# Performance work log

Measured on AMD Instinct MI355X. Metric: run time of the kernel, lower is better.

## Reference

```python
import math
import jax, jax.numpy as jnp
import numpy as np

B, T, E = 4, 2048, 768
H, D = 3, E // 3  # 3 heads, head_dim = emb_sz // 3
USE_MASK = True


def setup_inputs() -> dict:
    key = jax.random.key(0)
    ks = jax.random.split(key, 8)
    s_in = 1.0 / math.sqrt(E)
    return {
        "inputs_for_keys": jax.random.normal(ks[0], (B, T, E), jnp.float32),
        "inputs_for_values": jax.random.normal(ks[1], (B, T, E), jnp.float32),
        "inputs_for_queries": jax.random.normal(ks[2], (B, T, E), jnp.float32),
        # per-head projection weights, stacked over head axis: [H, E, D]
        "Wk": jax.random.normal(ks[3], (H, E, D), jnp.float32) * s_in,
        "Wq": jax.random.normal(ks[4], (H, E, D), jnp.float32) * s_in,
        "Wv": jax.random.normal(ks[5], (H, E, D), jnp.float32) * s_in,
        # final Dense(emb_sz)
        "Wo": jax.random.normal(ks[6], (E, E), jnp.float32) * s_in,
        "bo": jnp.zeros((E,), jnp.float32),
    }


def reference(inputs_for_keys, inputs_for_values, inputs_for_queries, Wk, Wq, Wv, Wo, bo):
    # Project per head: [B,T,E] x [H,E,D] -> [B,H,T,D]
    K = jnp.einsum('bte,hed->bhtd', inputs_for_keys, Wk)
    V = jnp.einsum('bte,hed->bhtd', inputs_for_values, Wv)
    Q = jnp.einsum('bte,hed->bhtd', inputs_for_queries, Wq)
    # NOTE: original scales by sqrt(window_size_keys) = sqrt(T), not sqrt(D)
    scores = jnp.einsum('bhqd,bhkd->bhqk', Q, K) / math.sqrt(T)
    if USE_MASK:
        mask = jnp.triu(jnp.full((T, T), -jnp.inf, dtype=scores.dtype), k=1)
        scores = scores + mask
    attn = jax.nn.softmax(scores, axis=-1)  # [B,H,Tq,Tk]
    z = jnp.einsum('bhqk,bhkd->bhqd', attn, V)  # [B,H,T,D]
    # concat heads in order head1,head2,head3 along last axis -> [B,T,E]
    z = jnp.transpose(z, (0, 2, 1, 3)).reshape(B, T, H * D)
    return z @ Wo + bo
```

## Files before the change

### kernel.cpp

```cpp
#include <hip/hip_runtime.h>
#include <hip/hip_bf16.h>
#include <math.h>

#define B_ 4
#define T_ 2048
#define E_ 768
#define H_ 3
#define D_ 256
#define LOG2E 1.4426950408889634f

typedef __attribute__((ext_vector_type(8))) _Float16 half8;
typedef __attribute__((ext_vector_type(8))) unsigned short ushort8;
typedef __attribute__((ext_vector_type(4))) float f32x4;

static __device__ inline unsigned short f2h(float x) {
    _Float16 h = (_Float16)x;
    return *reinterpret_cast<unsigned short*>(&h);
}

#define GLOAD_LDS(SRC, DST) \
    __builtin_amdgcn_global_load_lds( \
        (const __attribute__((address_space(1))) void*)(SRC), \
        (__attribute__((address_space(3))) void*)(DST), 16, 0, 0)

__global__ __launch_bounds__(256)
void transpose_cast_all(const float* __restrict__ Wk, const float* __restrict__ Wq,
                        const float* __restrict__ Wv, const float* __restrict__ Wo,
                        unsigned short* __restrict__ WTk, unsigned short* __restrict__ WTq,
                        unsigned short* __restrict__ WTv, unsigned short* __restrict__ WoT)
{
    __shared__ float tile[32][33];
    const int z = blockIdx.z;
    const float* in; unsigned short* out; int R, C;
    if (z < 9) {
        const int mat = z / 3, hd = z % 3;
        R = E_; C = D_;
        in  = (mat == 0 ? Wk  : mat == 1 ? Wq  : Wv)  + (long)hd * E_ * D_;
        out = (mat == 0 ? WTk : mat == 1 ? WTq : WTv) + (long)hd * D_ * E_;
    } else {
        R = E_; C = E_;
        in = Wo; out = WoT;
    }
    const int c0 = blockIdx.x * 32;
    const int r0 = blockIdx.y * 32;
    if (c0 >= C) return;
    const int t  = threadIdx.x;
    const int cc = t & 31, rr = t >> 5;
    #pragma unroll
    for (int i = 0; i < 4; ++i)
        tile[rr + i * 8][cc] = in[(long)(r0 + rr + i * 8) * C + c0 + cc];
    __syncthreads();
    const int rr2 = t & 31, cc2 = t >> 5;
    #pragma unroll
    for (int i = 0; i < 4; ++i)
        out[(long)(c0 + cc2 + i * 8) * R + r0 + rr2] = f2h(tile[rr2][cc2 + i * 8]);
}

__global__ __launch_bounds__(256)
void transpose16(const unsigned short* __restrict__ in, unsigned short* __restrict__ out,
                 int R, int Ccols)
{
    __shared__ unsigned short tile[64 * 64];
    char* tb = (char*)tile;
    const long zoff = (long)blockIdx.z * R * Ccols;
    const int r0 = blockIdx.y * 64, c0 = blockIdx.x * 64;
    const int t = threadIdx.x;
    #pragma unroll
    for (int i = 0; i < 2; ++i) {
        const int rr = (t >> 3) + i * 32;
        const int gc = (t & 7) * 8;
        ushort8 v = *(const ushort8*)(in + zoff + (long)(r0 + rr) * Ccols + c0 + gc);
        *(ushort8*)(tb + rr * 128 + ((gc * 2) ^ (((rr >> 3) & 7) << 4))) = v;
    }
    __syncthreads();
    #pragma unroll
    for (int i = 0; i < 2; ++i) {
        const int cc = (t >> 3) + i * 32;
        const int gr = (t & 7) * 8;
        ushort8 v;
        #pragma unroll
        for (int e = 0; e < 8; ++e) {
            const int row = gr + e;
            v[e] = *(const unsigned short*)(tb + row * 128 + ((cc * 2) ^ (((row >> 3) & 7) << 4)));
        }
        *(ushort8*)(out + zoff + (long)(c0 + cc) * R + r0 + gr) = v;
    }
}

template<bool CONVA, bool OUT16>
__device__ __forceinline__
void gemm_body(const float* Af, const unsigned short* Ah, const unsigned short* Bz,
               void* Cz, const float* bias, int K, int lda, int ldc,
               int m0, int n0, int tid)
{
    __shared__ unsigned short As[128 * 32];
    __shared__ unsigned short Bs[128 * 32];

    const int lane = tid & 63, wid = tid >> 6;
    const int wm = wid >> 1, wn = wid & 1;
    const int fr = lane & 15, fg = lane >> 4;

    f32x4 acc[4][4];
    #pragma unroll
    for (int mt = 0; mt < 4; ++mt)
        #pragma unroll
        for (int nt = 0; nt < 4; ++nt) acc[mt][nt] = (f32x4)(0.f);

    for (int k0 = 0; k0 < K; k0 += 32) {
        #pragma unroll
        for (int i = 0; i < 2; ++i) {
            const int G = tid + i * 256;
            const int row = G >> 2, g = G & 3;
            ushort8 pa;
            if (CONVA) {
                const float* s = Af + (long)(m0 + row) * lda + k0 + g * 8;
                float4 f0 = *(const float4*)s, f1 = *(const float4*)(s + 4);
                pa[0] = f2h(f0.x); pa[1] = f2h(f0.y); pa[2] = f2h(f0.z); pa[3] = f2h(f0.w);
                pa[4] = f2h(f1.x); pa[5] = f2h(f1.y); pa[6] = f2h(f1.z); pa[7] = f2h(f1.w);
            } else {
                pa = *(const ushort8*)(Ah + (long)(m0 + row) * lda + k0 + g * 8);
            }
            *(ushort8*)&As[row * 32 + g * 8] = pa;
            *(ushort8*)&Bs[row * 32 + g * 8] =
                *(const ushort8*)(Bz + (long)(n0 + row) * K + k0 + g * 8);
        }
        __syncthreads();

        half8 a[4], b[4];
        #pragma unroll
        for (int mt = 0; mt < 4; ++mt)
            a[mt] = *(const half8*)&As[(wm * 64 + mt * 16 + fr) * 32 + fg * 8];
        #pragma unroll
        for (int nt = 0; nt < 4; ++nt)
            b[nt] = *(const half8*)&Bs[(wn * 64 + nt * 16 + fr) * 32 + fg * 8];
        #pragma unroll
        for (int mt = 0; mt < 4; ++mt)
            #pragma unroll
            for (int nt = 0; nt < 4; ++nt)
                acc[mt][nt] = __builtin_amdgcn_mfma_f32_16x16x32_f16(
                                  a[mt], b[nt], acc[mt][nt], 0, 0, 0);
        __syncthreads();
    }

    #pragma unroll
    for (int nt = 0; nt < 4; ++nt) {
        const int col = n0 + wn * 64 + nt * 16 + fr;
        const float badd = bias ? bias[col] : 0.f;
        #pragma unroll
        for (int mt = 0; mt < 4; ++mt) {
            const int row = m0 + wm * 64 + mt * 16 + fg * 4;
            #pragma unroll
            for (int reg = 0; reg < 4; ++reg) {
                if (OUT16)
                    ((unsigned short*)Cz)[(long)(row + reg) * ldc + col] =
                        f2h(acc[mt][nt][reg] + badd);
                else
                    ((float*)Cz)[(long)(row + reg) * ldc + col] =
                        acc[mt][nt][reg] + badd;
            }
        }
    }
}

template<bool CONVA, bool OUT16>
__global__ __launch_bounds__(256)
void gemm_mfma(const void* __restrict__ Av, const unsigned short* __restrict__ Bt,
               void* __restrict__ Cv, const float* __restrict__ bias,
               int K, int Hdiv, int lda, int ldc, long sA, long sB, long sC)
{
    const int z = blockIdx.z;
    const float*          Af = (const float*)Av          + (long)(z / Hdiv) * sA;
    const unsigned short* Ah = (const unsigned short*)Av + (long)(z / Hdiv) * sA;
    const unsigned short* Bz = Bt + (long)(z % Hdiv) * sB;
    void* Cz = OUT16 ? (void*)((unsigned short*)Cv + (long)z * sC)
                     : (void*)((float*)Cv + (long)z * sC);
    gemm_body<CONVA, OUT16>(Af, Ah, Bz, Cz, bias, K, lda, ldc,
                            blockIdx.y * 128, blockIdx.x * 128, threadIdx.x);
}

__global__ __launch_bounds__(256)
void qkv_proj(const float* __restrict__ Xk, const float* __restrict__ Xv,
              const float* __restrict__ Xq,
              const unsigned short* __restrict__ WTk, const unsigned short* __restrict__ WTv,
              const unsigned short* __restrict__ WTq,
              unsigned short* __restrict__ Kp, unsigned short* __restrict__ Vp,
              unsigned short* __restrict__ Qp)
{
    const int z = blockIdx.z;
    const int which = z / 12, bh = z % 12;
    const int b = bh / H_, h = bh % H_;
    const float* X = (which == 0) ? Xk : (which == 1) ? Xv : Xq;
    const unsigned short* W = (which == 0) ? WTk : (which == 1) ? WTv : WTq;
    unsigned short* P = (which == 0) ? Kp : (which == 1) ? Vp : Qp;
    const float* Af = X + (long)b * T_ * E_;
    const unsigned short* Bz = W + (long)h * D_ * E_;
    unsigned short* Cz = P + (long)bh * T_ * D_;
    gemm_body<true, true>(Af, nullptr, Bz, Cz, nullptr, E_, E_, D_,
                          blockIdx.y * 128, blockIdx.x * 128, threadIdx.x);
}

__global__ __launch_bounds__(256, 2)
void flash_lds(const unsigned short* __restrict__ Qb, const unsigned short* __restrict__ Kb,
               const unsigned short* __restrict__ Vtb, unsigned short* __restrict__ Z2h,
               float scale_log2e)
{
    __shared__ unsigned short Ktile[2][32 * 256];
    __shared__ unsigned short Vtile[2][256 * 32];
    __shared__ unsigned short Ps[4][16 * 72];

    const int p  = blockIdx.x;
    const int bh = p % 12;
    const int pi = p / 12;
    const int qtB = 63 - pi;
    const int b = bh / H_, h = bh % H_;
    const int tid = threadIdx.x;
    const int w = tid >> 6, lane = tid & 63;
    const int g = lane >> 4, fr = lane & 15;
    const int qw0 = (w < 2) ? (pi * 32 + w * 16) : (qtB * 32 + (w - 2) * 16);

    const unsigned short* kg = Kb  + (long)bh * T_ * D_;
    const unsigned short* vg = Vtb + (long)bh * D_ * T_;

    const unsigned short* qrow = Qb + ((long)bh * T_ + qw0 + fr) * D_;
    const _Float16 hs = (_Float16)scale_log2e;
    half8 qf[8];
    #pragma unroll
    for (int c = 0; c < 8; ++c) {
        qf[c] = *(const half8*)(qrow + c * 32 + g * 8);
        qf[c] *= hs;
    }

    f32x4 o[16];
    #pragma unroll
    for (int dt = 0; dt < 16; ++dt) o[dt] = (f32x4)(0.f);
    float mrow[4] = {-INFINITY, -INFINITY, -INFINITY, -INFINITY};
    float lrow[4] = {0.f, 0.f, 0.f, 0.f};

    const int nkt = qtB + 1;

    auto STAGE = [&](int bufi, int kt) {
        const int k0 = kt * 32;
        #pragma unroll
        for (int i = 0; i < 4; ++i) {
            const int L = tid + i * 256;
            const int r = L >> 5, cg = L & 31;
            GLOAD_LDS(kg + (long)(k0 + r) * D_ + ((cg ^ (r & 7)) * 8),
                      &Ktile[bufi][L * 8]);
        }
        #pragma unroll
        for (int i = 0; i < 4; ++i) {
            const int L = tid + i * 256;
            const int dr = L >> 2, gq = L & 3;
            GLOAD_LDS(vg + (long)dr * T_ + k0 + ((gq ^ ((dr >> 1) & 3)) * 8),
                      &Vtile[bufi][L * 8]);
        }
    };

    STAGE(0, 0);
    int buf = 0;
    for (int kt = 0; kt < nkt; ++kt) {
        const bool pf = (kt + 1 < nkt);
        if (pf) {
            STAGE(buf ^ 1, kt + 1);
            asm volatile("s_waitcnt vmcnt(8)" ::: "memory");
        } else {
            asm volatile("s_waitcnt vmcnt(0)" ::: "memory");
        }
        __builtin_amdgcn_sched_barrier(0);
        __builtin_amdgcn_s_barrier();
        __builtin_amdgcn_sched_barrier(0);

        const int k0 = kt * 32;
        if (k0 <= qw0 + 15) {
            f32x4 s[2];
            s[0] = (f32x4)(0.f); s[1] = (f32x4)(0.f);
            const int kkey = fr & 7;
            __builtin_amdgcn_s_setprio(1);
            #pragma unroll
            for (int c = 0; c < 8; ++c) {
                #pragma unroll
                for (int nt = 0; nt < 2; ++nt) {
                    const int kr = nt * 16 + fr;
                    half8 kf = *(const half8*)&Ktile[buf][(kr * 32 + ((c * 4 + g) ^ kkey)) * 8];
                    s[nt] = __builtin_amdgcn_mfma_f32_16x16x32_f16(qf[c], kf, s[nt], 0, 0, 0);
                }
            }
            __builtin_amdgcn_s_setprio(0);

            const bool diag = (k0 + 31 > qw0);
            float sv[2][4];
            #pragma unroll
            for (int nt = 0; nt < 2; ++nt)
                #pragma unroll
                for (int reg = 0; reg < 4; ++reg) {
                    float v = s[nt][reg];
                    if (diag && (k0 + nt * 16 + fr > qw0 + g * 4 + reg)) v = -INFINITY;
                    sv[nt][reg] = v;
                }

            float pmax[4];
            #pragma unroll
            for (int reg = 0; reg < 4; ++reg) pmax[reg] = fmaxf(sv[0][reg], sv[1][reg]);
            const bool ok = (pmax[0] <= mrow[0] + 8.f) && (pmax[1] <= mrow[1] + 8.f)
                         && (pmax[2] <= mrow[2] + 8.f) && (pmax[3] <= mrow[3] + 8.f);
            if (!__all(ok)) {
                #pragma unroll
                for (int reg = 0; reg < 4; ++reg) {
                    float tm = pmax[reg];
                    tm = fmaxf(tm, __shfl_xor(tm, 1));
                    tm = fmaxf(tm, __shfl_xor(tm, 2));
                    tm = fmaxf(tm, __shfl_xor(tm, 4));
                    tm = fmaxf(tm, __shfl_xor(tm, 8));
                    const float mnew = fmaxf(mrow[reg], tm);
                    const float alpha = exp2f(mrow[reg] - mnew);
                    mrow[reg] = mnew;
                    lrow[reg] *= alpha;
                    #pragma unroll
                    for (int dt = 0; dt < 16; ++dt) o[dt][reg] *= alpha;
                }
            }
            #pragma unroll
            for (int nt = 0; nt < 2; ++nt)
                #pragma unroll
                for (int reg = 0; reg < 4; ++reg) {
                    const float pp = exp2f(sv[nt][reg] - mrow[reg]);
                    lrow[reg] += pp;
                    Ps[w][(g * 4 + reg) * 72 + nt * 16 + fr] = f2h(pp);
                }

            const half8 pf0 = *(const half8*)&Ps[w][fr * 72 + g * 8];

            const int vkey = g ^ ((fr >> 1) & 3);
            __builtin_amdgcn_s_setprio(1);
            #pragma unroll
            for (int dt = 0; dt < 16; ++dt) {
                const int dr = dt * 16 + fr;
                half8 vf = *(const half8*)&Vtile[buf][(dr * 4 + vkey) * 8];
                o[dt] = __builtin_amdgcn_mfma_f32_16x16x32_f16(pf0, vf, o[dt], 0, 0, 0);
            }
            __builtin_amdgcn_s_setprio(0);
        }
        __builtin_amdgcn_sched_barrier(0);
        __builtin_amdgcn_s_barrier();
        buf ^= 1;
    }

    float inv[4];
    #pragma unroll
    for (int reg = 0; reg < 4; ++reg) {
        float ps = lrow[reg];
        ps += __shfl_xor(ps, 1);
        ps += __shfl_xor(ps, 2);
        ps += __shfl_xor(ps, 4);
        ps += __shfl_xor(ps, 8);
        inv[reg] = 1.f / ps;
    }
    const long rowbase = ((long)b * T_ + qw0 + g * 4) * E_ + h * D_;
    #pragma unroll
    for (int reg = 0; reg < 4; ++reg) {
        unsigned short* dst = Z2h + rowbase + (long)reg * E_ + fr;
        #pragma unroll
        for (int dt = 0; dt < 16; ++dt)
            dst[dt * 16] = f2h(o[dt][reg] * inv[reg]);
    }
}

extern "C" void kernel_launch(void* const* d_in, const int* in_sizes, int n_in,
                              void* d_out, int out_size, void* d_ws, size_t ws_size,
                              hipStream_t stream)
{
    const float* Xk = (const float*)d_in[0];
    const float* Xv = (const float*)d_in[1];
    const float* Xq = (const float*)d_in[2];
    const float* Wk = (const float*)d_in[3];
    const float* Wq = (const float*)d_in[4];
    const float* Wv = (const float*)d_in[5];
    const float* Wo = (const float*)d_in[6];
    const float* bo = (const float*)d_in[7];
    float* out = (float*)d_out;

    const size_t phd = (size_t)B_ * H_ * T_ * D_;
    const size_t wsz = (size_t)H_ * E_ * D_;
    unsigned short* Kp  = (unsigned short*)d_ws;
    unsigned short* Vp  = Kp + phd;
    unsigned short* Qp  = Vp + phd;
    unsigned short* Vt  = Qp + phd;
    unsigned short* Z2h = Vt + phd;
    unsigned short* WTk = Z2h + (size_t)B_ * T_ * E_;
    unsigned short* WTq = WTk + wsz;
    unsigned short* WTv = WTq + wsz;
    unsigned short* WoT = WTv + wsz;

    dim3 blk(256);

    dim3 gtw(E_ / 32, E_ / 32, 10);
    transpose_cast_all<<<gtw, blk, 0, stream>>>(Wk, Wq, Wv, Wo, WTk, WTq, WTv, WoT);

    dim3 gproj(D_ / 128, T_ / 128, 36);
    qkv_proj<<<gproj, blk, 0, stream>>>(Xk, Xv, Xq, WTk, WTv, WTq, Kp, Vp, Qp);

    dim3 gtv(D_ / 64, T_ / 64, B_ * H_);
    transpose16<<<gtv, blk, 0, stream>>>(Vp, Vt, T_, D_);

    dim3 gf(32 * B_ * H_);
    flash_lds<<<gf, blk, 0, stream>>>(Qp, Kp, Vt, Z2h,
                                      0.022097086912079608f * LOG2E);

    dim3 gout(E_ / 128, (B_ * T_) / 128, 1);
    gemm_mfma<false, false><<<gout, blk, 0, stream>>>(Z2h, WoT, out, bo, E_, 1, E_, E_,
                                                      0L, 0L, 0L);
}
```

Before: 202.2 us.

## Process two 16-row query subtiles per wave in flash attention

Each wave now computes attention for 32 query rows, as two 16-row subtiles, instead of 16. Every K and V fragment read from LDS feeds two MFMAs, which halves LDS read traffic per unit of compute and halves the number of K/V tile loads from global memory. The grid shrinks to 192 blocks, and the block index is remapped so blocks sharing a batch-head land on the same XCD. In exchange, each thread holds twice the accumulator registers and launch bounds drop to one block per CU, so fewer blocks than CUs run and there is less latency hiding.

```diff
diff --git a/kernel.cpp b/kernel.cpp
--- a/kernel.cpp
+++ b/kernel.cpp
@@ -199,44 +199,52 @@
                           blockIdx.y * 128, blockIdx.x * 128, threadIdx.x);
 }
 
-__global__ __launch_bounds__(256, 2)
-void flash_lds(const unsigned short* __restrict__ Qb, const unsigned short* __restrict__ Kb,
-               const unsigned short* __restrict__ Vtb, unsigned short* __restrict__ Z2h,
-               float scale_log2e)
+__global__ __launch_bounds__(256, 1)
+void flash_dual(const unsigned short* __restrict__ Qb, const unsigned short* __restrict__ Kb,
+                const unsigned short* __restrict__ Vtb, unsigned short* __restrict__ Z2h,
+                float scale_log2e)
 {
     __shared__ unsigned short Ktile[2][32 * 256];
     __shared__ unsigned short Vtile[2][256 * 32];
     __shared__ unsigned short Ps[4][16 * 72];
 
     const int p  = blockIdx.x;
-    const int bh = p % 12;
-    const int pi = p / 12;
-    const int qtB = 63 - pi;
+    const int l  = (p & 7) * 24 + (p >> 3);
+    const int bh = l >> 4;
+    const int pi = l & 15;
     const int b = bh / H_, h = bh % H_;
     const int tid = threadIdx.x;
     const int w = tid >> 6, lane = tid & 63;
     const int g = lane >> 4, fr = lane & 15;
-    const int qw0 = (w < 2) ? (pi * 32 + w * 16) : (qtB * 32 + (w - 2) * 16);
+    const int base = (w < 2) ? (pi * 64 + w * 32) : ((31 - pi) * 64 + (w - 2) * 32);
 
     const unsigned short* kg = Kb  + (long)bh * T_ * D_;
     const unsigned short* vg = Vtb + (long)bh * D_ * T_;
 
-    const unsigned short* qrow = Qb + ((long)bh * T_ + qw0 + fr) * D_;
     const _Float16 hs = (_Float16)scale_log2e;
-    half8 qf[8];
-    #pragma unroll
-    for (int c = 0; c < 8; ++c) {
-        qf[c] = *(const half8*)(qrow + c * 32 + g * 8);
-        qf[c] *= hs;
-    }
-
-    f32x4 o[16];
-    #pragma unroll
-    for (int dt = 0; dt < 16; ++dt) o[dt] = (f32x4)(0.f);
-    float mrow[4] = {-INFINITY, -INFINITY, -INFINITY, -INFINITY};
-    float lrow[4] = {0.f, 0.f, 0.f, 0.f};
-
-    const int nkt = qtB + 1;
+    half8 qf[2][8];
+    #pragma unroll
+    for (int st = 0; st < 2; ++st) {
+        const unsigned short* qrow = Qb + ((long)bh * T_ + base + st * 16 + fr) * D_;
+        #pragma unroll
+        for (int c = 0; c < 8; ++c) {
+            qf[st][c] = *(const half8*)(qrow + c * 32 + g * 8);
+            qf[st][c] *= hs;
+        }
+    }
+
+    f32x4 o[2][16];
+    #pragma unroll
+    for (int st = 0; st < 2; ++st)
+        #pragma unroll
+        for (int dt = 0; dt < 16; ++dt) o[st][dt] = (f32x4)(0.f);
+    float mrow[2][4], lrow[2][4];
+    #pragma unroll
+    for (int st = 0; st < 2; ++st)
+        #pragma unroll
+        for (int reg = 0; reg < 4; ++reg) { mrow[st][reg] = -INFINITY; lrow[st][reg] = 0.f; }
+
+    const int nkt = 2 * (31 - pi) + 2;
 
     auto STAGE = [&](int bufi, int kt) {
         const int k0 = kt * 32;
@@ -259,8 +267,8 @@
     STAGE(0, 0);
     int buf = 0;
     for (int kt = 0; kt < nkt; ++kt) {
-        const bool pf = (kt + 1 < nkt);
-        if (pf) {
+        const bool pf_ = (kt + 1 < nkt);
+        if (pf_) {
             STAGE(buf ^ 1, kt + 1);
             asm volatile("s_waitcnt vmcnt(8)" ::: "memory");
         } else {
@@ -271,9 +279,10 @@
         __builtin_amdgcn_sched_barrier(0);
 
         const int k0 = kt * 32;
-        if (k0 <= qw0 + 15) {
-            f32x4 s[2];
-            s[0] = (f32x4)(0.f); s[1] = (f32x4)(0.f);
+        if (k0 <= base + 31) {
+            f32x4 sA[2], sB[2];
+            sA[0] = (f32x4)(0.f); sA[1] = (f32x4)(0.f);
+            sB[0] = (f32x4)(0.f); sB[1] = (f32x4)(0.f);
             const int kkey = fr & 7;
             __builtin_amdgcn_s_setprio(1);
             #pragma unroll
@@ -282,53 +291,64 @@
                 for (int nt = 0; nt < 2; ++nt) {
                     const int kr = nt * 16 + fr;
                     half8 kf = *(const half8*)&Ktile[buf][(kr * 32 + ((c * 4 + g) ^ kkey)) * 8];
-                    s[nt] = __builtin_amdgcn_mfma_f32_16x16x32_f16(qf[c], kf, s[nt], 0, 0, 0);
+                    sA[nt] = __builtin_amdgcn_mfma_f32_16x16x32_f16(qf[0][c], kf, sA[nt], 0, 0, 0);
+                    sB[nt] = __builtin_amdgcn_mfma_f32_16x16x32_f16(qf[1][c], kf, sB[nt], 0, 0, 0);
                 }
             }
             __builtin_amdgcn_s_setprio(0);
 
-            const bool diag = (k0 + 31 > qw0);
-            float sv[2][4];
             #pragma unroll
             for (int nt = 0; nt < 2; ++nt)
                 #pragma unroll
                 for (int reg = 0; reg < 4; ++reg) {
-                    float v = s[nt][reg];
-                    if (diag && (k0 + nt * 16 + fr > qw0 + g * 4 + reg)) v = -INFINITY;
-                    sv[nt][reg] = v;
+                    const int kk = k0 + nt * 16 + fr;
+                    if ((k0 + 31 > base)      && (kk > base + g * 4 + reg))      sA[nt][reg] = -INFINITY;
+                    if ((k0 + 31 > base + 16) && (kk > base + 16 + g * 4 + reg)) sB[nt][reg] = -INFINITY;
                 }
 
-            float pmax[4];
-            #pragma unroll
-            for (int reg = 0; reg < 4; ++reg) pmax[reg] = fmaxf(sv[0][reg], sv[1][reg]);
-            const bool ok = (pmax[0] <= mrow[0] + 8.f) && (pmax[1] <= mrow[1] + 8.f)
-                         && (pmax[2] <= mrow[2] + 8.f) && (pmax[3] <= mrow[3] + 8.f);
+            float pmA[4], pmB[4];
+            #pragma unroll
+            for (int reg = 0; reg < 4; ++reg) {
+                pmA[reg] = fmaxf(sA[0][reg], sA[1][reg]);
+                pmB[reg] = fmaxf(sB[0][reg], sB[1][reg]);
+            }
+            const bool ok = (pmA[0] <= mrow[0][0] + 8.f) && (pmA[1] <= mrow[0][1] + 8.f)
+                         && (pmA[2] <= mrow[0][2] + 8.f) && (pmA[3] <= mrow[0][3] + 8.f)
+                         && (pmB[0] <= mrow[1][0] + 8.f) && (pmB[1] <= mrow[1][1] + 8.f)
+                         && (pmB[2] <= mrow[1][2] + 8.f) && (pmB[3] <= mrow[1][3] + 8.f);
             if (!__all(ok)) {
                 #pragma unroll
-                for (int reg = 0; reg < 4; ++reg) {
-                    float tm = pmax[reg];
-                    tm = fmaxf(tm, __shfl_xor(tm, 1));
-                    tm = fmaxf(tm, __shfl_xor(tm, 2));
-                    tm = fmaxf(tm, __shfl_xor(tm, 4));
-                    tm = fmaxf(tm, __shfl_xor(tm, 8));
-                    const float mnew = fmaxf(mrow[reg], tm);
-                    const float alpha = exp2f(mrow[reg] - mnew);
-                    mrow[reg] = mnew;
-                    lrow[reg] *= alpha;
+                for (int st = 0; st < 2; ++st)
                     #pragma unroll
-                    for (int dt = 0; dt < 16; ++dt) o[dt][reg] *= alpha;
-                }
-            }
-            #pragma unroll
-            for (int nt = 0; nt < 2; ++nt)
+                    for (int reg = 0; reg < 4; ++reg) {
+                        float tm = st ? pmB[reg] : pmA[reg];
+                        tm = fmaxf(tm, __shfl_xor(tm, 1));
+                        tm = fmaxf(tm, __shfl_xor(tm, 2));
+                        tm = fmaxf(tm, __shfl_xor(tm, 4));
+                        tm = fmaxf(tm, __shfl_xor(tm, 8));
+                        const float mnew = fmaxf(mrow[st][reg], tm);
+                        const float alpha = exp2f(mrow[st][reg] - mnew);
+                        mrow[st][reg] = mnew;
+                        lrow[st][reg] *= alpha;
+                        #pragma unroll
+                        for (int dt = 0; dt < 16; ++dt) o[st][dt][reg] *= alpha;
+                    }
+            }
+
+            half8 pfr[2];
+            #pragma unroll
+            for (int st = 0; st < 2; ++st) {
                 #pragma unroll
-                for (int reg = 0; reg < 4; ++reg) {
-                    const float pp = exp2f(sv[nt][reg] - mrow[reg]);
-                    lrow[reg] += pp;
-                    Ps[w][(g * 4 + reg) * 72 + nt * 16 + fr] = f2h(pp);
-                }
-
-            const half8 pf0 = *(const half8*)&Ps[w][fr * 72 + g * 8];
+                for (int nt = 0; nt < 2; ++nt)
+                    #pragma unroll
+                    for (int reg = 0; reg < 4; ++reg) {
+                        const float svv = st ? sB[nt][reg] : sA[nt][reg];
+                        const float pp = exp2f(svv - mrow[st][reg]);
+                        lrow[st][reg] += pp;
+                        Ps[w][(g * 4 + reg) * 72 + nt * 16 + fr] = f2h(pp);
+                    }
+                pfr[st] = *(const half8*)&Ps[w][fr * 72 + g * 8];
+            }
 
             const int vkey = g ^ ((fr >> 1) & 3);
             __builtin_amdgcn_s_setprio(1);
@@ -336,7 +356,8 @@
             for (int dt = 0; dt < 16; ++dt) {
                 const int dr = dt * 16 + fr;
                 half8 vf = *(const half8*)&Vtile[buf][(dr * 4 + vkey) * 8];
-                o[dt] = __builtin_amdgcn_mfma_f32_16x16x32_f16(pf0, vf, o[dt], 0, 0, 0);
+                o[0][dt] = __builtin_amdgcn_mfma_f32_16x16x32_f16(pfr[0], vf, o[0][dt], 0, 0, 0);
+                o[1][dt] = __builtin_amdgcn_mfma_f32_16x16x32_f16(pfr[1], vf, o[1][dt], 0, 0, 0);
             }
             __builtin_amdgcn_s_setprio(0);
         }
@@ -345,23 +366,26 @@
         buf ^= 1;
     }
 
-    float inv[4];
-    #pragma unroll
-    for (int reg = 0; reg < 4; ++reg) {
-        float ps = lrow[reg];
-        ps += __shfl_xor(ps, 1);
-        ps += __shfl_xor(ps, 2);
-        ps += __shfl_xor(ps, 4);
-        ps += __shfl_xor(ps, 8);
-        inv[reg] = 1.f / ps;
-    }
-    const long rowbase = ((long)b * T_ + qw0 + g * 4) * E_ + h * D_;
-    #pragma unroll
-    for (int reg = 0; reg < 4; ++reg) {
-        unsigned short* dst = Z2h + rowbase + (long)reg * E_ + fr;
-        #pragma unroll
-        for (int dt = 0; dt < 16; ++dt)
-            dst[dt * 16] = f2h(o[dt][reg] * inv[reg]);
+    #pragma unroll
+    for (int st = 0; st < 2; ++st) {
+        float inv[4];
+        #pragma unroll
+        for (int reg = 0; reg < 4; ++reg) {
+            float ps = lrow[st][reg];
+            ps += __shfl_xor(ps, 1);
+            ps += __shfl_xor(ps, 2);
+            ps += __shfl_xor(ps, 4);
+            ps += __shfl_xor(ps, 8);
+            inv[reg] = 1.f / ps;
+        }
+        const long rowbase = ((long)b * T_ + base + st * 16 + g * 4) * E_ + h * D_;
+        #pragma unroll
+        for (int reg = 0; reg < 4; ++reg) {
+            unsigned short* dst = Z2h + rowbase + (long)reg * E_ + fr;
+            #pragma unroll
+            for (int dt = 0; dt < 16; ++dt)
+                dst[dt * 16] = f2h(o[st][dt][reg] * inv[reg]);
+        }
     }
 }
 
@@ -402,9 +426,9 @@
     dim3 gtv(D_ / 64, T_ / 64, B_ * H_);
     transpose16<<<gtv, blk, 0, stream>>>(Vp, Vt, T_, D_);
 
-    dim3 gf(32 * B_ * H_);
-    flash_lds<<<gf, blk, 0, stream>>>(Qp, Kp, Vt, Z2h,
-                                      0.022097086912079608f * LOG2E);
+    dim3 gf(16 * B_ * H_);
+    flash_dual<<<gf, blk, 0, stream>>>(Qp, Kp, Vt, Z2h,
+                                       0.022097086912079608f * LOG2E);
 
     dim3 gout(E_ / 128, (B_ * T_) / 128, 1);
     gemm_mfma<false, false><<<gout, blk, 0, stream>>>(Z2h, WoT, out, bo, E_, 1, E_, E_,
```

After: 251.4 us. +24.3%, slower.
